# Kernel tuning notes

Hardware: AMD Instinct MI355X
Metric: run time of the kernel (lower is better)

## Reference

```python
import jax, jax.numpy as jnp
import numpy as np

B, S, H = 4, 16, 4096          # batch, new query tokens, hidden
NH, NKV, HD = 32, 8, 128       # query heads, kv heads, head_dim
PAST = 8192                    # cached kv length
ROPE_BASE = 10000.0


def setup_inputs() -> dict:
    key = jax.random.key(0)
    ks = jax.random.split(key, 7)
    wscale = 0.02
    hidden_states = jax.random.normal(ks[0], (B, S, H), jnp.float32)
    k_cache = jax.random.normal(ks[1], (B, PAST, NKV, HD), jnp.float32)
    v_cache = jax.random.normal(ks[2], (B, PAST, NKV, HD), jnp.float32)
    Wq = jax.random.normal(ks[3], (H, NH * HD), jnp.float32) * wscale
    Wk = jax.random.normal(ks[4], (H, NKV * HD), jnp.float32) * wscale
    Wv = jax.random.normal(ks[5], (H, NKV * HD), jnp.float32) * wscale
    Wo = jax.random.normal(ks[6], (NH * HD, H), jnp.float32) * wscale
    position_ids = PAST + jnp.tile(jnp.arange(S, dtype=jnp.int32)[None, :], (B, 1))
    return {"hidden_states": hidden_states, "k_cache": k_cache, "v_cache": v_cache,
            "Wq": Wq, "Wk": Wk, "Wv": Wv, "Wo": Wo, "position_ids": position_ids}


def _rotate_half(x):
    h = x.shape[-1] // 2
    return jnp.concatenate([-x[..., h:], x[..., :h]], axis=-1)


def reference(hidden_states, k_cache, v_cache, Wq, Wk, Wv, Wo, position_ids):
    b, s, _ = hidden_states.shape
    # projections -> [b, heads, s, hd]
    q = (hidden_states @ Wq).reshape(b, s, NH, HD).transpose(0, 2, 1, 3)
    k = (hidden_states @ Wk).reshape(b, s, NKV, HD).transpose(0, 2, 1, 3)
    v = (hidden_states @ Wv).reshape(b, s, NKV, HD).transpose(0, 2, 1, 3)
    # RoPE (LlamaRotaryEmbedding: base=10000, half-split rotate)
    inv_freq = 1.0 / (ROPE_BASE ** (jnp.arange(0, HD, 2, dtype=jnp.float32) / HD))
    ang = position_ids.astype(jnp.float32)[..., None] * inv_freq      # [b, s, hd/2]
    emb = jnp.concatenate([ang, ang], axis=-1)                        # [b, s, hd]
    cos = jnp.cos(emb)[:, None]                                       # [b, 1, s, hd]
    sin = jnp.sin(emb)[:, None]
    q = q * cos + _rotate_half(q) * sin
    k = k * cos + _rotate_half(k) * sin
    # kv-cache concat: cache stored [b, past, nkv, hd] -> [b, nkv, K, hd]
    k_all = jnp.concatenate([k_cache.transpose(0, 2, 1, 3), k], axis=2)
    v_all = jnp.concatenate([v_cache.transpose(0, 2, 1, 3), v], axis=2)
    # GQA repeat_kv (repeat_interleave along head dim)
    n_rep = NH // NKV
    k_all = jnp.repeat(k_all, n_rep, axis=1)                          # [b, NH, K, hd]
    v_all = jnp.repeat(v_all, n_rep, axis=1)
    K = k_all.shape[2]
    scale = HD ** -0.5
    scores = jnp.einsum('bhqd,bhkd->bhqk', q, k_all) * scale          # [b, NH, s, K]
    # flash varlen causal with seqlen_q < seqlen_k: bottom-right aligned mask
    allow = jnp.arange(K)[None, :] <= (K - s + jnp.arange(s))[:, None]
    scores = jnp.where(allow, scores, jnp.float32(-1e30))
    probs = jax.nn.softmax(scores, axis=-1)
    attn = jnp.einsum('bhqk,bhkd->bhqd', probs, v_all)                # [b, NH, s, hd]
    attn = attn.transpose(0, 2, 1, 3).reshape(b, s, NH * HD)
    return attn @ Wo
```

## Files before the change

### kernel.cpp

```cpp
#include <hip/hip_runtime.h>

#define BB 4
#define SS 16
#define NH 32
#define NKV 8
#define HD 128
#define PAST 8192
#define KVLEN 8208
#define KSPLIT 8
#define ASPLIT 16
#define CHUNK 513

typedef __attribute__((ext_vector_type(8))) short short8;
typedef __attribute__((ext_vector_type(4))) float f32x4;

__device__ __forceinline__ unsigned short f2bf(float f) {
  unsigned u = __float_as_uint(f);
  u = (u + 0x7FFFu + ((u >> 16) & 1u)) >> 16;
  return (unsigned short)u;
}
__device__ __forceinline__ float bf2f(unsigned short h) {
  return __uint_as_float(((unsigned)h) << 16);
}
__device__ __forceinline__ float getc(const float4& v, int c) {
  return c == 0 ? v.x : c == 1 ? v.y : c == 2 ? v.z : v.w;
}

__device__ __forceinline__ void bar_lds() {
  asm volatile("s_waitcnt lgkmcnt(0)" ::: "memory");
  __builtin_amdgcn_s_barrier();
  asm volatile("" ::: "memory");
}
__device__ __forceinline__ void wait_lds() {
  asm volatile("s_waitcnt lgkmcnt(0)" ::: "memory");
}

__global__ __launch_bounds__(256) void xconv(const float* __restrict__ X,
                                             unsigned short* __restrict__ XB) {
  int gid = blockIdx.x * 256 + threadIdx.x;
  float4 v = *(const float4*)&X[(size_t)gid * 4];
  ushort4 pk;
  pk.x = f2bf(v.x); pk.y = f2bf(v.y); pk.z = f2bf(v.z); pk.w = f2bf(v.w);
  *(ushort4*)&XB[(size_t)gid * 4] = pk;
}

__global__ __launch_bounds__(256) void gemm_skinny(
    const unsigned short* __restrict__ A,
    const float* __restrict__ W0, const float* __restrict__ W1, const float* __restrict__ W2,
    int nw0, int nw1, int nw2,
    float* __restrict__ part, int Ntot, int kchunk) {
  __shared__ unsigned short Wt[64 * 64];
  const int nt = blockIdx.x, ks = blockIdx.y;
  const int tid = threadIdx.x, lane = tid & 63, w = tid >> 6;
  const int lr = lane & 15, lc = lane >> 4;
  const int n0 = nt * 64;
  const float* W; int wld, wcol;
  if (n0 < nw0) { W = W0; wld = nw0; wcol = n0; }
  else if (n0 < nw0 + nw1) { W = W1; wld = nw1; wcol = n0 - nw0; }
  else { W = W2; wld = nw2; wcol = n0 - nw0 - nw1; }

  f32x4 acc[4];
  #pragma unroll
  for (int mi = 0; mi < 4; ++mi)
    #pragma unroll
    for (int i = 0; i < 4; ++i) acc[mi][i] = 0.f;

  const int qn = tid & 15, qk = tid >> 4;
  const int kb0 = ks * kchunk;
  const int nkt = kchunk / 64;

  float4 wr0, wr1, wr2, wr3;
  {
    const float* wp = &W[(size_t)(kb0 + qk * 4) * wld + wcol + qn * 4];
    wr0 = *(const float4*)(wp);
    wr1 = *(const float4*)(wp + wld);
    wr2 = *(const float4*)(wp + 2 * (size_t)wld);
    wr3 = *(const float4*)(wp + 3 * (size_t)wld);
  }

  for (int kt = 0; kt < nkt; ++kt) {
    const int kb = kb0 + kt * 64;
    #pragma unroll
    for (int c = 0; c < 4; ++c) {
      const int n = qn * 4 + c;
      ushort4 pk;
      pk.x = f2bf(getc(wr0, c)); pk.y = f2bf(getc(wr1, c));
      pk.z = f2bf(getc(wr2, c)); pk.w = f2bf(getc(wr3, c));
      const int byt = n * 128 + ((qk * 8) ^ ((n & 7) << 4));
      *(ushort4*)((char*)Wt + byt) = pk;
    }
    bar_lds();
    if (kt + 1 < nkt) {
      const float* wp = &W[(size_t)(kb + 64 + qk * 4) * wld + wcol + qn * 4];
      wr0 = *(const float4*)(wp);
      wr1 = *(const float4*)(wp + wld);
      wr2 = *(const float4*)(wp + 2 * (size_t)wld);
      wr3 = *(const float4*)(wp + 3 * (size_t)wld);
    }
    #pragma unroll
    for (int kh = 0; kh < 2; ++kh) {
      const int ncol = w * 16 + lr;
      short8 bf = *(const short8*)((char*)Wt + ncol * 128 + ((kh * 64 + lc * 16) ^ ((ncol & 7) << 4)));
      const int kkg = kb + kh * 32 + lc * 8;
      #pragma unroll
      for (int mi = 0; mi < 4; ++mi) {
        short8 af = *(const short8*)&A[(size_t)(mi * 16 + lr) * 4096 + kkg];
        acc[mi] = __builtin_amdgcn_mfma_f32_16x16x32_bf16(af, bf, acc[mi], 0, 0, 0);
      }
    }
    bar_lds();
  }
  #pragma unroll
  for (int mi = 0; mi < 4; ++mi)
    #pragma unroll
    for (int i = 0; i < 4; ++i) {
      const int row = mi * 16 + lc * 4 + i;
      part[((size_t)ks * 64 + row) * Ntot + n0 + w * 16 + lr] = acc[mi][i];
    }
}

__global__ __launch_bounds__(256) void proj_reduce(
    const float* __restrict__ part, const int* __restrict__ posids,
    unsigned short* __restrict__ QR, float* __restrict__ KF,
    float* __restrict__ VF) {
  const int gid = blockIdx.x * 256 + threadIdx.x;
  const int j = gid & 63;
  const int hh = (gid >> 6) % 48;
  const int row = gid / 3072;
  const int b = row >> 4, s = row & 15;
  int col0; bool rope;
  if (hh < 32)      { col0 = hh * 128 + j; rope = true; }
  else if (hh < 40) { col0 = 4096 + (hh - 32) * 128 + j; rope = true; }
  else              { col0 = 5120 + (hh - 40) * 128 + j; rope = false; }
  float v0 = 0.f, v1 = 0.f;
  #pragma unroll
  for (int ks = 0; ks < KSPLIT; ++ks) {
    v0 += part[((size_t)ks * 64 + row) * 6144 + col0];
    v1 += part[((size_t)ks * 64 + row) * 6144 + col0 + 64];
  }
  float o0 = v0, o1 = v1;
  if (rope) {
    const int pos = posids[row];
    const double inv = exp2(-(double)j * (13.287712379549449 / 64.0));
    double th = (double)pos * inv;
    const double TWO_PI = 6.283185307179586476925286766559;
    th -= floor(th / TWO_PI) * TWO_PI;
    float sv, cv;
    sincosf((float)th, &sv, &cv);
    o0 = v0 * cv - v1 * sv;
    o1 = v1 * cv + v0 * sv;
  }
  if (hh < 32) {
    const size_t didx = (((size_t)(b * 32 + hh) * 16 + s) * 128) + j;
    QR[didx] = f2bf(o0);
    QR[didx + 64] = f2bf(o1);
  } else if (hh < 40) {
    const size_t didx = (((size_t)(b * 8 + (hh - 32)) * 16 + s) * 128) + j;
    KF[didx] = o0;
    KF[didx + 64] = o1;
  } else {
    const size_t didx = (((size_t)(b * 8 + (hh - 40)) * 16 + s) * 128) + j;
    VF[didx] = o0;
    VF[didx + 64] = o1;
  }
}

__global__ __launch_bounds__(256, 2) void attn_kernel(
    const float* __restrict__ kc, const float* __restrict__ vc,
    const unsigned short* __restrict__ QR, const float* __restrict__ KF,
    const float* __restrict__ VF,
    float* __restrict__ Opart, float* __restrict__ ML) {
  __shared__ unsigned short Klds[64 * 136];
  __shared__ unsigned short Vt[128 * 64];
  __shared__ unsigned short Plds[4][16 * 72];

  const int split = blockIdx.x, kvh = blockIdx.y, b = blockIdx.z;
  const int tid = threadIdx.x, lane = tid & 63, w = tid >> 6;
  const int lr = lane & 15, lc = lane >> 4;

  short8 qf[4];
  {
    const unsigned short* qb = QR + (((size_t)b * NH + kvh * 4 + w) * SS + lr) * HD;
    #pragma unroll
    for (int kd = 0; kd < 4; ++kd) qf[kd] = *(const short8*)(qb + kd * 32 + lc * 8);
  }

  float m_i[4], l_i[4];
  f32x4 oacc[8];
  #pragma unroll
  for (int i = 0; i < 4; ++i) { m_i[i] = -1e30f; l_i[i] = 0.f; }
  #pragma unroll
  for (int d8 = 0; d8 < 8; ++d8)
    #pragma unroll
    for (int i = 0; i < 4; ++i) oacc[d8][i] = 0.f;

  const int kstart = split * CHUNK;
  const int dl = (tid & 31) * 4;
  const int rk = tid >> 5;

  const float* kc_base = kc + (((size_t)b * PAST) * NKV + kvh) * HD + dl;
  const float* vc_base = vc + (((size_t)b * PAST) * NKV + kvh) * HD + dl;
  const float* kf_base = KF + (((size_t)b * NKV + kvh) * SS) * HD + dl;
  const float* vf_base = VF + (((size_t)b * NKV + kvh) * SS) * HD + dl;

  float4 kpre[8];
  float4 vpre[2][4];

  auto load_tile = [&](int kk0) {
    #pragma unroll
    for (int pass = 0; pass < 8; ++pass) {
      const int kr = pass * 8 + rk;
      const int kk = kk0 + kr;
      int ts = kk - PAST;
      ts = ts < 0 ? 0 : (ts > SS - 1 ? SS - 1 : ts);
      const float* p = (kk < PAST) ? (kc_base + (size_t)kk * (NKV * HD))
                                   : (kf_base + (size_t)ts * HD);
      kpre[pass] = *(const float4*)p;
    }
    #pragma unroll
    for (int pp = 0; pp < 2; ++pp)
      #pragma unroll
      for (int jj = 0; jj < 4; ++jj) {
        const int kr = rk * 8 + pp * 4 + jj;
        const int kk = kk0 + kr;
        int ts = kk - PAST;
        ts = ts < 0 ? 0 : (ts > SS - 1 ? SS - 1 : ts);
        const float* p = (kk < PAST) ? (vc_base + (size_t)kk * (NKV * HD))
                                     : (vf_base + (size_t)ts * HD);
        vpre[pp][jj] = *(const float4*)p;
      }
  };

  auto store_tile = [&]() {
    #pragma unroll
    for (int pass = 0; pass < 8; ++pass) {
      const int kr = pass * 8 + rk;
      const float4 f = kpre[pass];
      ushort4 pk;
      pk.x = f2bf(f.x); pk.y = f2bf(f.y); pk.z = f2bf(f.z); pk.w = f2bf(f.w);
      *(ushort4*)((char*)Klds + kr * 272 + dl * 2) = pk;
    }
    #pragma unroll
    for (int pp = 0; pp < 2; ++pp) {
      const int krb = rk * 8 + pp * 4;
      #pragma unroll
      for (int c = 0; c < 4; ++c) {
        const int d = dl + c;
        const int g = ((d ^ (d >> 3)) & 7) << 4;
        ushort4 pk;
        pk.x = f2bf(getc(vpre[pp][0], c));
        pk.y = f2bf(getc(vpre[pp][1], c));
        pk.z = f2bf(getc(vpre[pp][2], c));
        pk.w = f2bf(getc(vpre[pp][3], c));
        *(ushort4*)((char*)Vt + d * 128 + ((krb * 2) ^ g)) = pk;
      }
    }
  };

  load_tile(kstart);

  for (int t = 0; t < 9; ++t) {
    const int kk0 = kstart + t * 64;
    const int nvalid = min(64, kstart + CHUNK - kk0);

    store_tile();
    bar_lds();

    if (t < 8) load_tile(kk0 + 64);

    f32x4 sacc[4];
    #pragma unroll
    for (int nb = 0; nb < 4; ++nb)
      #pragma unroll
      for (int i = 0; i < 4; ++i) sacc[nb][i] = 0.f;
    #pragma unroll
    for (int kd = 0; kd < 4; ++kd) {
      #pragma unroll
      for (int nb = 0; nb < 4; ++nb) {
        const int key = nb * 16 + lr;
        short8 bf = *(const short8*)((char*)Klds + key * 272 + kd * 64 + lc * 16);
        sacc[nb] = __builtin_amdgcn_mfma_f32_16x16x32_bf16(qf[kd], bf, sacc[nb], 0, 0, 0);
      }
    }

    const float scl = 0.08838834764831845f;
    float resc[4];
    #pragma unroll
    for (int i = 0; i < 4; ++i) {
      const int s = lc * 4 + i;
      float vv[4];
      #pragma unroll
      for (int nb = 0; nb < 4; ++nb) {
        const int klocal = nb * 16 + lr;
        const int kk = kk0 + klocal;
        const bool ok = (klocal < nvalid) && (kk <= PAST + s);
        vv[nb] = ok ? sacc[nb][i] * scl : -1e30f;
      }
      float mx = fmaxf(fmaxf(vv[0], vv[1]), fmaxf(vv[2], vv[3]));
      mx = fmaxf(mx, __shfl_xor(mx, 1));
      mx = fmaxf(mx, __shfl_xor(mx, 2));
      mx = fmaxf(mx, __shfl_xor(mx, 4));
      mx = fmaxf(mx, __shfl_xor(mx, 8));
      const float mnew = fmaxf(m_i[i], mx);
      const float rs = __expf(m_i[i] - mnew);
      float p0 = __expf(vv[0] - mnew), p1 = __expf(vv[1] - mnew);
      float p2 = __expf(vv[2] - mnew), p3 = __expf(vv[3] - mnew);
      float sum = p0 + p1 + p2 + p3;
      sum += __shfl_xor(sum, 1);
      sum += __shfl_xor(sum, 2);
      sum += __shfl_xor(sum, 4);
      sum += __shfl_xor(sum, 8);
      l_i[i] = l_i[i] * rs + sum;
      m_i[i] = mnew;
      resc[i] = rs;
      unsigned short* prow = &Plds[w][s * 72];
      prow[0 * 16 + lr] = f2bf(p0);
      prow[1 * 16 + lr] = f2bf(p1);
      prow[2 * 16 + lr] = f2bf(p2);
      prow[3 * 16 + lr] = f2bf(p3);
    }
    #pragma unroll
    for (int d8 = 0; d8 < 8; ++d8)
      #pragma unroll
      for (int i = 0; i < 4; ++i) oacc[d8][i] *= resc[i];

    wait_lds();

    #pragma unroll
    for (int ks2 = 0; ks2 < 2; ++ks2) {
      short8 pf = *(const short8*)((char*)&Plds[w][0] + lr * 144 + ks2 * 64 + lc * 16);
      #pragma unroll
      for (int db = 0; db < 8; ++db) {
        const int d = db * 16 + lr;
        const int g = ((d ^ (d >> 3)) & 7) << 4;
        short8 vf = *(const short8*)((char*)Vt + d * 128 + ((ks2 * 64 + lc * 16) ^ g));
        oacc[db] = __builtin_amdgcn_mfma_f32_16x16x32_bf16(pf, vf, oacc[db], 0, 0, 0);
      }
    }
    bar_lds();
  }

  const size_t pbase = (((size_t)b * NKV + kvh) * ASPLIT + split) * 64;
  #pragma unroll
  for (int db = 0; db < 8; ++db)
    #pragma unroll
    for (int i = 0; i < 4; ++i) {
      const int row = w * 16 + lc * 4 + i;
      Opart[(pbase + row) * HD + db * 16 + lr] = oacc[db][i];
    }
  if (lr == 0) {
    #pragma unroll
    for (int i = 0; i < 4; ++i) {
      const int row = w * 16 + lc * 4 + i;
      ML[(pbase + row) * 2] = m_i[i];
      ML[(pbase + row) * 2 + 1] = l_i[i];
    }
  }
}

__global__ __launch_bounds__(128) void combine(const float* __restrict__ Opart,
                                               const float* __restrict__ ML,
                                               unsigned short* __restrict__ AT) {
  const int rid = blockIdx.x;
  const int d = threadIdx.x;
  const int s = rid & 15, h = (rid >> 4) & 31, b = rid >> 9;
  const int kvh = h >> 2, g = h & 3;
  const int prow = g * 16 + s;
  const size_t base = ((size_t)b * NKV + kvh) * ASPLIT;
  float ms[ASPLIT], ls[ASPLIT];
  float M = -1e30f;
  #pragma unroll
  for (int sp = 0; sp < ASPLIT; ++sp) {
    ms[sp] = ML[((base + sp) * 64 + prow) * 2];
    ls[sp] = ML[((base + sp) * 64 + prow) * 2 + 1];
    M = fmaxf(M, ms[sp]);
  }
  float denom = 0.f, acc = 0.f;
  #pragma unroll
  for (int sp = 0; sp < ASPLIT; ++sp) {
    const float e = __expf(ms[sp] - M);
    denom += ls[sp] * e;
    acc += e * Opart[((base + sp) * 64 + prow) * HD + d];
  }
  AT[((size_t)(b * 16 + s)) * 4096 + h * 128 + d] = f2bf(acc / denom);
}

__global__ __launch_bounds__(256) void wo_reduce(const float* __restrict__ part,
                                                 float* __restrict__ out) {
  const int gid = blockIdx.x * 256 + threadIdx.x;
  float4 s = {0, 0, 0, 0};
  #pragma unroll
  for (int ks = 0; ks < KSPLIT; ++ks) {
    const float4 v = *(const float4*)&part[(size_t)ks * 262144 + (size_t)gid * 4];
    s.x += v.x; s.y += v.y; s.z += v.z; s.w += v.w;
  }
  *(float4*)&out[(size_t)gid * 4] = s;
}

extern "C" void kernel_launch(void* const* d_in, const int* in_sizes, int n_in,
                              void* d_out, int out_size, void* d_ws, size_t ws_size,
                              hipStream_t stream) {
  (void)in_sizes; (void)n_in; (void)out_size; (void)ws_size;
  const float* hs = (const float*)d_in[0];
  const float* kc = (const float*)d_in[1];
  const float* vc = (const float*)d_in[2];
  const float* Wq = (const float*)d_in[3];
  const float* Wk = (const float*)d_in[4];
  const float* Wv = (const float*)d_in[5];
  const float* Wo = (const float*)d_in[6];
  const int* pos = (const int*)d_in[7];
  float* out = (float*)d_out;
  char* ws = (char*)d_ws;

  unsigned short* XB = (unsigned short*)(ws);
  unsigned short* QR = (unsigned short*)(ws + 0x080000);
  float* KF = (float*)(ws + 0x100000);
  float* VF = (float*)(ws + 0x140000);
  unsigned short* AT = (unsigned short*)(ws + 0x180000);
  float* RED = (float*)(ws + 0x200000);
  float* ML  = (float*)(ws + 0x1300000);

  hipLaunchKernelGGL(xconv, dim3(256), dim3(256), 0, stream, hs, XB);
  hipLaunchKernelGGL(gemm_skinny, dim3(96, KSPLIT), dim3(256), 0, stream,
                     XB, Wq, Wk, Wv, 4096, 1024, 1024, RED, 6144, 4096 / KSPLIT);
  hipLaunchKernelGGL(proj_reduce, dim3(768), dim3(256), 0, stream, RED, pos, QR, KF, VF);
  hipLaunchKernelGGL(attn_kernel, dim3(ASPLIT, NKV, BB), dim3(256), 0, stream,
                     kc, vc, QR, KF, VF, RED, ML);
  hipLaunchKernelGGL(combine, dim3(2048), dim3(128), 0, stream, RED, ML, AT);
  hipLaunchKernelGGL(gemm_skinny, dim3(64, KSPLIT), dim3(256), 0, stream,
                     AT, Wo, Wo, Wo, 4096, 0, 0, RED, 4096, 4096 / KSPLIT);
  hipLaunchKernelGGL(wo_reduce, dim3(256), dim3(256), 0, stream, RED, out);
}
```

Baseline: 138.8 us.

## Stream fp32 KV tiles via async global_load_lds double buffering in attention

Measured after the change: 187.7 us. 1.35x slower.

```diff
diff --git a/kernel.cpp b/kernel.cpp
--- a/kernel.cpp
+++ b/kernel.cpp
@@ -8,8 +8,9 @@
 #define PAST 8192
 #define KVLEN 8208
 #define KSPLIT 8
-#define ASPLIT 16
-#define CHUNK 513
+#define NSPLIT 18
+#define NTILE 15
+#define TK 32
 
 typedef __attribute__((ext_vector_type(8))) short short8;
 typedef __attribute__((ext_vector_type(4))) float f32x4;
@@ -22,6 +23,9 @@
 __device__ __forceinline__ float bf2f(unsigned short h) {
   return __uint_as_float(((unsigned)h) << 16);
 }
+__device__ __forceinline__ unsigned pk2bf(float a, float b) {
+  return (unsigned)f2bf(a) | ((unsigned)f2bf(b) << 16);
+}
 __device__ __forceinline__ float getc(const float4& v, int c) {
   return c == 0 ? v.x : c == 1 ? v.y : c == 2 ? v.z : v.w;
 }
@@ -34,6 +38,11 @@
 __device__ __forceinline__ void wait_lds() {
   asm volatile("s_waitcnt lgkmcnt(0)" ::: "memory");
 }
+
+#define GLOAD16(gsrc, ldst)                                                        \
+  __builtin_amdgcn_global_load_lds(                                                \
+      (const __attribute__((address_space(1))) void*)(gsrc),                       \
+      (__attribute__((address_space(3))) void*)(ldst), 16, 0, 0)
 
 __global__ __launch_bounds__(256) void xconv(const float* __restrict__ X,
                                              unsigned short* __restrict__ XB) {
@@ -170,9 +179,9 @@
     const unsigned short* __restrict__ QR, const float* __restrict__ KF,
     const float* __restrict__ VF,
     float* __restrict__ Opart, float* __restrict__ ML) {
-  __shared__ unsigned short Klds[64 * 136];
-  __shared__ unsigned short Vt[128 * 64];
-  __shared__ unsigned short Plds[4][16 * 72];
+  __shared__ float Kf[2][TK * HD];
+  __shared__ float Vf[2][TK * HD];
+  __shared__ unsigned short Pl[4][16 * 40];
 
   const int split = blockIdx.x, kvh = blockIdx.y, b = blockIdx.z;
   const int tid = threadIdx.x, lane = tid & 63, w = tid >> 6;
@@ -194,92 +203,66 @@
     #pragma unroll
     for (int i = 0; i < 4; ++i) oacc[d8][i] = 0.f;
 
-  const int kstart = split * CHUNK;
-  const int dl = (tid & 31) * 4;
-  const int rk = tid >> 5;
-
-  const float* kc_base = kc + (((size_t)b * PAST) * NKV + kvh) * HD + dl;
-  const float* vc_base = vc + (((size_t)b * PAST) * NKV + kvh) * HD + dl;
-  const float* kf_base = KF + (((size_t)b * NKV + kvh) * SS) * HD + dl;
-  const float* vf_base = VF + (((size_t)b * NKV + kvh) * SS) * HD + dl;
-
-  float4 kpre[8];
-  float4 vpre[2][4];
-
-  auto load_tile = [&](int kk0) {
-    #pragma unroll
-    for (int pass = 0; pass < 8; ++pass) {
-      const int kr = pass * 8 + rk;
-      const int kk = kk0 + kr;
-      int ts = kk - PAST;
-      ts = ts < 0 ? 0 : (ts > SS - 1 ? SS - 1 : ts);
-      const float* p = (kk < PAST) ? (kc_base + (size_t)kk * (NKV * HD))
-                                   : (kf_base + (size_t)ts * HD);
-      kpre[pass] = *(const float4*)p;
-    }
-    #pragma unroll
-    for (int pp = 0; pp < 2; ++pp)
-      #pragma unroll
-      for (int jj = 0; jj < 4; ++jj) {
-        const int kr = rk * 8 + pp * 4 + jj;
-        const int kk = kk0 + kr;
-        int ts = kk - PAST;
-        ts = ts < 0 ? 0 : (ts > SS - 1 ? SS - 1 : ts);
-        const float* p = (kk < PAST) ? (vc_base + (size_t)kk * (NKV * HD))
-                                     : (vf_base + (size_t)ts * HD);
-        vpre[pp][jj] = *(const float4*)p;
-      }
+  const int kbase = split * (NTILE * TK);
+
+  const int rA = lane >> 5;
+  const int cpr = lane & 31;
+  const float* kc_blk = kc + ((size_t)b * PAST * NKV + kvh) * HD;
+  const float* vc_blk = vc + ((size_t)b * PAST * NKV + kvh) * HD;
+  const float* kf_blk = KF + (((size_t)b * NKV + kvh) * SS) * HD;
+  const float* vf_blk = VF + (((size_t)b * NKV + kvh) * SS) * HD;
+
+  auto issue_tile = [&](int t, int buf) {
+    const int kk0 = kbase + t * TK;
+    #pragma unroll
+    for (int p = 0; p < 4; ++p) {
+      const int row = (w * 4 + p) * 2 + rA;
+      const int sw = (row & 7) ^ (((row >> 3) & 3) << 1);
+      const int d0 = (cpr ^ sw) << 2;
+      const int kk = kk0 + row;
+      const int ts = min(max(kk - PAST, 0), SS - 1);
+      const float* sK = (kk < PAST) ? (kc_blk + (size_t)kk * (NKV * HD) + d0)
+                                    : (kf_blk + (size_t)ts * HD + d0);
+      GLOAD16(sK, &Kf[buf][(w * 4 + p) * 256]);
+    }
+    #pragma unroll
+    for (int p = 0; p < 4; ++p) {
+      const int row = (w * 4 + p) * 2 + rA;
+      const int sw = (row & 7) ^ (((row >> 3) & 3) << 1);
+      const int d0 = (cpr ^ sw) << 2;
+      const int kk = kk0 + row;
+      const int ts = min(max(kk - PAST, 0), SS - 1);
+      const float* sV = (kk < PAST) ? (vc_blk + (size_t)kk * (NKV * HD) + d0)
+                                    : (vf_blk + (size_t)ts * HD + d0);
+      GLOAD16(sV, &Vf[buf][(w * 4 + p) * 256]);
+    }
   };
 
-  auto store_tile = [&]() {
-    #pragma unroll
-    for (int pass = 0; pass < 8; ++pass) {
-      const int kr = pass * 8 + rk;
-      const float4 f = kpre[pass];
-      ushort4 pk;
-      pk.x = f2bf(f.x); pk.y = f2bf(f.y); pk.z = f2bf(f.z); pk.w = f2bf(f.w);
-      *(ushort4*)((char*)Klds + kr * 272 + dl * 2) = pk;
-    }
-    #pragma unroll
-    for (int pp = 0; pp < 2; ++pp) {
-      const int krb = rk * 8 + pp * 4;
-      #pragma unroll
-      for (int c = 0; c < 4; ++c) {
-        const int d = dl + c;
-        const int g = ((d ^ (d >> 3)) & 7) << 4;
-        ushort4 pk;
-        pk.x = f2bf(getc(vpre[pp][0], c));
-        pk.y = f2bf(getc(vpre[pp][1], c));
-        pk.z = f2bf(getc(vpre[pp][2], c));
-        pk.w = f2bf(getc(vpre[pp][3], c));
-        *(ushort4*)((char*)Vt + d * 128 + ((krb * 2) ^ g)) = pk;
-      }
-    }
-  };
-
-  load_tile(kstart);
-
-  for (int t = 0; t < 9; ++t) {
-    const int kk0 = kstart + t * 64;
-    const int nvalid = min(64, kstart + CHUNK - kk0);
-
-    store_tile();
-    bar_lds();
-
-    if (t < 8) load_tile(kk0 + 64);
-
-    f32x4 sacc[4];
-    #pragma unroll
-    for (int nb = 0; nb < 4; ++nb)
+  auto compute_tile = [&](int t, int buf) {
+    const int kk0 = kbase + t * TK;
+    const int nvalid = min(TK, max(0, KVLEN - kk0));
+    const float* Kb = &Kf[buf][0];
+    const float* Vb = &Vf[buf][0];
+
+    f32x4 sacc[2];
+    #pragma unroll
+    for (int nb = 0; nb < 2; ++nb)
       #pragma unroll
       for (int i = 0; i < 4; ++i) sacc[nb][i] = 0.f;
     #pragma unroll
-    for (int kd = 0; kd < 4; ++kd) {
+    for (int nb = 0; nb < 2; ++nb) {
+      const int key = nb * 16 + lr;
+      const int sw = (key & 7) ^ (((key >> 3) & 3) << 1);
+      const float* kr = Kb + key * HD;
       #pragma unroll
-      for (int nb = 0; nb < 4; ++nb) {
-        const int key = nb * 16 + lr;
-        short8 bf = *(const short8*)((char*)Klds + key * 272 + kd * 64 + lc * 16);
-        sacc[nb] = __builtin_amdgcn_mfma_f32_16x16x32_bf16(qf[kd], bf, sacc[nb], 0, 0, 0);
+      for (int kd = 0; kd < 4; ++kd) {
+        const int c0 = kd * 8 + lc * 2;
+        const float4 fA = *(const float4*)(kr + ((c0 ^ sw) << 2));
+        const float4 fB = *(const float4*)(kr + (((c0 + 1) ^ sw) << 2));
+        union { unsigned u[4]; short8 v; } tm;
+        tm.u[0] = pk2bf(fA.x, fA.y); tm.u[1] = pk2bf(fA.z, fA.w);
+        tm.u[2] = pk2bf(fB.x, fB.y); tm.u[3] = pk2bf(fB.z, fB.w);
+        sacc[nb] = __builtin_amdgcn_mfma_f32_16x16x32_bf16(qf[kd], tm.v, sacc[nb], 0, 0, 0);
       }
     }
 
@@ -288,24 +271,20 @@
     #pragma unroll
     for (int i = 0; i < 4; ++i) {
       const int s = lc * 4 + i;
-      float vv[4];
-      #pragma unroll
-      for (int nb = 0; nb < 4; ++nb) {
-        const int klocal = nb * 16 + lr;
-        const int kk = kk0 + klocal;
-        const bool ok = (klocal < nvalid) && (kk <= PAST + s);
-        vv[nb] = ok ? sacc[nb][i] * scl : -1e30f;
-      }
-      float mx = fmaxf(fmaxf(vv[0], vv[1]), fmaxf(vv[2], vv[3]));
+      const int k0 = kk0 + lr, k1 = kk0 + 16 + lr;
+      const bool ok0 = (lr < nvalid) && (k0 <= PAST + s);
+      const bool ok1 = (16 + lr < nvalid) && (k1 <= PAST + s);
+      float vv0 = ok0 ? sacc[0][i] * scl : -1e30f;
+      float vv1 = ok1 ? sacc[1][i] * scl : -1e30f;
+      float mx = fmaxf(vv0, vv1);
       mx = fmaxf(mx, __shfl_xor(mx, 1));
       mx = fmaxf(mx, __shfl_xor(mx, 2));
       mx = fmaxf(mx, __shfl_xor(mx, 4));
       mx = fmaxf(mx, __shfl_xor(mx, 8));
       const float mnew = fmaxf(m_i[i], mx);
       const float rs = __expf(m_i[i] - mnew);
-      float p0 = __expf(vv[0] - mnew), p1 = __expf(vv[1] - mnew);
-      float p2 = __expf(vv[2] - mnew), p3 = __expf(vv[3] - mnew);
-      float sum = p0 + p1 + p2 + p3;
+      float p0 = __expf(vv0 - mnew), p1 = __expf(vv1 - mnew);
+      float sum = p0 + p1;
       sum += __shfl_xor(sum, 1);
       sum += __shfl_xor(sum, 2);
       sum += __shfl_xor(sum, 4);
@@ -313,11 +292,9 @@
       l_i[i] = l_i[i] * rs + sum;
       m_i[i] = mnew;
       resc[i] = rs;
-      unsigned short* prow = &Plds[w][s * 72];
-      prow[0 * 16 + lr] = f2bf(p0);
-      prow[1 * 16 + lr] = f2bf(p1);
-      prow[2 * 16 + lr] = f2bf(p2);
-      prow[3 * 16 + lr] = f2bf(p3);
+      unsigned short* prow = &Pl[w][s * 40];
+      prow[lr] = f2bf(p0);
+      prow[16 + lr] = f2bf(p1);
     }
     #pragma unroll
     for (int d8 = 0; d8 < 8; ++d8)
@@ -326,21 +303,48 @@
 
     wait_lds();
 
-    #pragma unroll
-    for (int ks2 = 0; ks2 < 2; ++ks2) {
-      short8 pf = *(const short8*)((char*)&Plds[w][0] + lr * 144 + ks2 * 64 + lc * 16);
+    short8 pf = *(const short8*)&Pl[w][lr * 40 + lc * 8];
+    int swv[8];
+    #pragma unroll
+    for (int j = 0; j < 8; ++j) swv[j] = j ^ (lc << 1);
+    #pragma unroll
+    for (int db = 0; db < 8; ++db) {
+      const int cb = db * 4 + (lr >> 2);
+      float fj[8];
       #pragma unroll
-      for (int db = 0; db < 8; ++db) {
-        const int d = db * 16 + lr;
-        const int g = ((d ^ (d >> 3)) & 7) << 4;
-        short8 vf = *(const short8*)((char*)Vt + d * 128 + ((ks2 * 64 + lc * 16) ^ g));
-        oacc[db] = __builtin_amdgcn_mfma_f32_16x16x32_bf16(pf, vf, oacc[db], 0, 0, 0);
+      for (int j = 0; j < 8; ++j) {
+        const int key = lc * 8 + j;
+        fj[j] = Vb[(size_t)key * HD + (((cb ^ swv[j]) << 2) + (lr & 3))];
       }
-    }
-    bar_lds();
-  }
-
-  const size_t pbase = (((size_t)b * NKV + kvh) * ASPLIT + split) * 64;
+      union { unsigned u[4]; short8 v; } tv;
+      tv.u[0] = pk2bf(fj[0], fj[1]); tv.u[1] = pk2bf(fj[2], fj[3]);
+      tv.u[2] = pk2bf(fj[4], fj[5]); tv.u[3] = pk2bf(fj[6], fj[7]);
+      oacc[db] = __builtin_amdgcn_mfma_f32_16x16x32_bf16(pf, tv.v, oacc[db], 0, 0, 0);
+    }
+  };
+
+  issue_tile(0, 0);
+  issue_tile(1, 1);
+  asm volatile("s_waitcnt vmcnt(8)" ::: "memory");
+  __builtin_amdgcn_s_barrier();
+  asm volatile("" ::: "memory");
+
+  for (int t = 0; t < NTILE; ++t) {
+    const int buf = t & 1;
+    compute_tile(t, buf);
+    __builtin_amdgcn_s_barrier();
+    asm volatile("" ::: "memory");
+    if (t < NTILE - 2) {
+      issue_tile(t + 2, buf);
+      asm volatile("s_waitcnt vmcnt(8)" ::: "memory");
+    } else {
+      asm volatile("s_waitcnt vmcnt(0)" ::: "memory");
+    }
+    __builtin_amdgcn_s_barrier();
+    asm volatile("" ::: "memory");
+  }
+
+  const size_t pbase = (((size_t)b * NKV + kvh) * NSPLIT + split) * 64;
   #pragma unroll
   for (int db = 0; db < 8; ++db)
     #pragma unroll
@@ -366,18 +370,18 @@
   const int s = rid & 15, h = (rid >> 4) & 31, b = rid >> 9;
   const int kvh = h >> 2, g = h & 3;
   const int prow = g * 16 + s;
-  const size_t base = ((size_t)b * NKV + kvh) * ASPLIT;
-  float ms[ASPLIT], ls[ASPLIT];
+  const size_t base = ((size_t)b * NKV + kvh) * NSPLIT;
+  float ms[NSPLIT], ls[NSPLIT];
   float M = -1e30f;
   #pragma unroll
-  for (int sp = 0; sp < ASPLIT; ++sp) {
+  for (int sp = 0; sp < NSPLIT; ++sp) {
     ms[sp] = ML[((base + sp) * 64 + prow) * 2];
     ls[sp] = ML[((base + sp) * 64 + prow) * 2 + 1];
     M = fmaxf(M, ms[sp]);
   }
   float denom = 0.f, acc = 0.f;
   #pragma unroll
-  for (int sp = 0; sp < ASPLIT; ++sp) {
+  for (int sp = 0; sp < NSPLIT; ++sp) {
     const float e = __expf(ms[sp] - M);
     denom += ls[sp] * e;
     acc += e * Opart[((base + sp) * 64 + prow) * HD + d];
@@ -418,13 +422,13 @@
   float* VF = (float*)(ws + 0x140000);
   unsigned short* AT = (unsigned short*)(ws + 0x180000);
   float* RED = (float*)(ws + 0x200000);
-  float* ML  = (float*)(ws + 0x1300000);
+  float* ML  = (float*)(ws + 0x1600000);
 
   hipLaunchKernelGGL(xconv, dim3(256), dim3(256), 0, stream, hs, XB);
   hipLaunchKernelGGL(gemm_skinny, dim3(96, KSPLIT), dim3(256), 0, stream,
                      XB, Wq, Wk, Wv, 4096, 1024, 1024, RED, 6144, 4096 / KSPLIT);
   hipLaunchKernelGGL(proj_reduce, dim3(768), dim3(256), 0, stream, RED, pos, QR, KF, VF);
-  hipLaunchKernelGGL(attn_kernel, dim3(ASPLIT, NKV, BB), dim3(256), 0, stream,
+  hipLaunchKernelGGL(attn_kernel, dim3(NSPLIT, NKV, BB), dim3(256), 0, stream,
                      kc, vc, QR, KF, VF, RED, ML);
   hipLaunchKernelGGL(combine, dim3(2048), dim3(128), 0, stream, RED, ML, AT);
   hipLaunchKernelGGL(gemm_skinny, dim3(64, KSPLIT), dim3(256), 0, stream,
```
